# Kernel optimization log

Measured on AMD Instinct MI355X. Metric: run time of the kernel, lower is better.

## Reference

```python
import jax, jax.numpy as jnp
import numpy as np

B, T, F, H, L = 512, 512, 64, 128, 3


def setup_inputs() -> dict:
    key = jax.random.key(0)
    ks = jax.random.split(key, 6)
    s_in = 1.0 / np.sqrt(F)
    s_h = 1.0 / np.sqrt(H)
    return {
        "x": jax.random.normal(ks[0], (B, T, F), dtype=jnp.float32),
        "Wx0": jax.random.normal(ks[1], (F, 3 * H), dtype=jnp.float32) * s_in,
        "Wx_rest": jax.random.normal(ks[2], (L - 1, H, 3 * H), dtype=jnp.float32) * s_h,
        "Wh": jax.random.normal(ks[3], (L, H, 3 * H), dtype=jnp.float32) * s_h,
        "b": jnp.zeros((L, 3 * H), dtype=jnp.float32),
        "Wd": jax.random.normal(ks[4], (H, H), dtype=jnp.float32) * s_h,
        "bd": jnp.zeros((H,), dtype=jnp.float32),
    }


def _gru_layer(x_seq, Wx, Wh_l, b_l):
    """x_seq: [T, B, Din] -> [T, B, H]. Classic GRU (reset_after=False)."""
    # Precompute input projections for all timesteps in one GEMM: [T, B, 3H]
    gx = jnp.einsum("tbd,dg->tbg", x_seq, Wx) + b_l

    def step(h, gx_t):
        gh = h @ Wh_l                      # [B, 3H]
        xz, xr, xn = jnp.split(gx_t, 3, axis=-1)
        hz, hr, hn = jnp.split(gh, 3, axis=-1)
        z = jax.nn.sigmoid(xz + hz)
        r = jax.nn.sigmoid(xr + hr)
        n = jnp.tanh(xn + r * hn)
        h_new = z * h + (1.0 - z) * n
        return h_new, h_new

    h0 = jnp.zeros((x_seq.shape[1], Wh_l.shape[0]), dtype=x_seq.dtype)
    _, hs = jax.lax.scan(step, h0, gx)
    return hs                              # [T, B, H]


def reference(x, Wx0, Wx_rest, Wh, b, Wd, bd):
    h = jnp.swapaxes(x, 0, 1)              # [T, B, F] time-major for scan
    h = _gru_layer(h, Wx0, Wh[0], b[0])
    for l in range(1, L):                  # small fixed layer loop
        h = _gru_layer(h, Wx_rest[l - 1], Wh[l], b[l])
    h = jnp.swapaxes(h, 0, 1)              # [B, T, H]
    return jax.nn.sigmoid(jnp.einsum("bth,hk->btk", h, Wd) + bd)
```

## Files before the change

### kernel.cpp

```cpp
#include <hip/hip_runtime.h>

namespace {

constexpr int Bb = 512, Tt = 512, Ff = 64, Hh = 128, Gg = 384;
constexpr int CH = 64;
constexpr int NCH = Tt / CH;

using short8  = __attribute__((ext_vector_type(8))) short;
using short4v = __attribute__((ext_vector_type(4))) short;
using f32x4   = __attribute__((ext_vector_type(4))) float;

__device__ __forceinline__ short f2bf(float f) {
  unsigned u = __float_as_uint(f);
  u += 0x7FFFu + ((u >> 16) & 1u);
  return (short)(u >> 16);
}
__device__ __forceinline__ float bf2f(short s) {
  return __uint_as_float(((unsigned)(unsigned short)s) << 16);
}
__device__ __forceinline__ float sigm(float x) { return 1.0f / (1.0f + __expf(-x)); }
__device__ __forceinline__ float tanh_fast(float x) { return 1.0f - 2.0f / (1.0f + __expf(2.0f * x)); }

__device__ __forceinline__ void gl_lds16(const char* g, char* l) {
  __builtin_amdgcn_global_load_lds((const __attribute__((address_space(1))) void*)g,
                                   (__attribute__((address_space(3))) void*)l, 16, 0, 0);
}

__global__ __launch_bounds__(512, 4) void prep(const float* __restrict__ Wx0,
                                               const float* __restrict__ Wxr,
                                               const float* __restrict__ Wh,
                                               const float* __restrict__ Wd,
                                               char* __restrict__ WhF,
                                               char* __restrict__ WxF,
                                               char* __restrict__ WdF) {
  const int id = blockIdx.x * 512 + threadIdx.x;
  const int lane = id & 63, lr = lane & 15, lk = lane >> 4;
  const int q = id >> 6;
  const float* src; int col, ldn, row0; char* dst;
  if (q < 288) {
    const int l = q / 96, rem = q % 96, w = rem / 12, f = rem % 12;
    const int g = f >> 2, ks = f & 3;
    src = Wh + (size_t)l * Hh * Gg; ldn = Gg;
    col = g * 128 + w * 16 + lr; row0 = ks * 32 + lk * 8;
    dst = WhF + (size_t)(q * 64 + lane) * 16;
  } else if (q < 528) {
    int p = q - 288; int base;
    if (p < 48)       { src = Wx0; base = 0; }
    else if (p < 144) { src = Wxr; base = 48; p -= 48; }
    else              { src = Wxr + (size_t)Hh * Gg; base = 144; p -= 144; }
    int ct, ks;
    if (base == 0) { ct = p >> 1; ks = p & 1; } else { ct = p >> 2; ks = p & 3; }
    ldn = Gg; col = ct * 16 + lr; row0 = ks * 32 + lk * 8;
    dst = WxF + (size_t)((base + p) * 64 + lane) * 16;
  } else {
    const int p = q - 528;
    const int ct = p >> 2, ks = p & 3;
    src = Wd; ldn = Hh; col = ct * 16 + lr; row0 = ks * 32 + lk * 8;
    dst = WdF + (size_t)(p * 64 + lane) * 16;
  }
  short8 v;
#pragma unroll
  for (int j = 0; j < 8; ++j) v[j] = f2bf(src[(size_t)(row0 + j) * ldn + col]);
  *(short8*)dst = v;
}

template <int KS>
__device__ void gemm_chunk(const void* __restrict__ src, int t0,
                           const char* __restrict__ wxf,
                           const float* __restrict__ bias,
                           char* __restrict__ gx, int wg, char* at) {
  constexpr int ROWB = KS * 64;
  const int tid = threadIdx.x;
  const int w = tid >> 6, lane = tid & 63, lr = lane & 15, lk = lane >> 4;
  const int trel = wg >> 3, b0 = (wg & 7) * 64;

  if constexpr (KS == 2) {
    const float* x = (const float*)src;
    const int row = tid >> 3, seg = tid & 7;
    const float* pr = x + ((size_t)(b0 + row) * Tt + t0 + trel) * Ff + seg * 8;
    f32x4 a = *(const f32x4*)pr, c = *(const f32x4*)(pr + 4);
    short8 o;
#pragma unroll
    for (int j = 0; j < 4; ++j) { o[j] = f2bf(a[j]); o[4 + j] = f2bf(c[j]); }
    *(short8*)(at + row * ROWB + ((seg * 16) ^ ((row & 7) << 4))) = o;
  } else {
    const char* h = (const char*)src + ((size_t)trel * 512 + b0) * ROWB;
    gl_lds16(h + tid * 16, at + tid * 16);
    gl_lds16(h + 8192 + tid * 16, at + 8192 + tid * 16);
    asm volatile("s_waitcnt vmcnt(0)");
  }
  __syncthreads();

  short8 bw[3][KS];
  f32x4 bs4[3];
#pragma unroll
  for (int c = 0; c < 3; ++c) {
    const int ct = w * 3 + c;
    bs4[c] = *(const f32x4*)(bias + ct * 16 + lk * 4);
#pragma unroll
    for (int ks = 0; ks < KS; ++ks)
      bw[c][ks] = *(const short8*)(wxf + (size_t)((ct * KS + ks) * 64 + lane) * 16);
  }

#pragma unroll
  for (int rt = 0; rt < 4; ++rt) {
    const int row = rt * 16 + lr;
    short8 aa[KS];
#pragma unroll
    for (int ks = 0; ks < KS; ++ks)
      aa[ks] = *(const short8*)(at + row * ROWB + ((ks * 64 + lk * 16) ^ ((row & 7) << 4)));
#pragma unroll
    for (int c = 0; c < 3; ++c) {
      f32x4 acc = {0.f, 0.f, 0.f, 0.f};
#pragma unroll
      for (int ks = 0; ks < KS; ++ks)
        acc = __builtin_amdgcn_mfma_f32_16x16x32_bf16(bw[c][ks], aa[ks], acc, 0, 0, 0);
      const int ct = w * 3 + c;
      short4v o;
#pragma unroll
      for (int i = 0; i < 4; ++i) o[i] = f2bf(acc[i] + bs4[c][i]);
      const int rb = (b0 >> 4) + rt;
      *(short4v*)(gx + (size_t)((trel * 32 + rb) * 8 + (ct & 7)) * 1536 + lane * 24 + (ct >> 3) * 8) = o;
    }
  }
}

template <bool DENSE>
__device__ void scan_chunk(const char* __restrict__ gx,
                           const char* __restrict__ whf,
                           short* __restrict__ hstream,
                           float* __restrict__ state, int t0,
                           const char* __restrict__ wdf,
                           const float* __restrict__ bdp,
                           float* __restrict__ out, int rb,
                           char* h_buf, float* ob) {
  const int tid = threadIdx.x;
  const int w = tid >> 6, lane = tid & 63, lr = lane & 15, lk = lane >> 4;

  short8 bwh[3][4];
#pragma unroll
  for (int g = 0; g < 3; ++g)
#pragma unroll
    for (int ks = 0; ks < 4; ++ks)
      bwh[g][ks] = *(const short8*)(whf + (size_t)((w * 12 + g * 4 + ks) * 64 + lane) * 16);

  short8 bwd[4];
  f32x4 bd4 = {0.f, 0.f, 0.f, 0.f};
  if constexpr (DENSE) {
#pragma unroll
    for (int ks = 0; ks < 4; ++ks)
      bwd[ks] = *(const short8*)(wdf + (size_t)((w * 4 + ks) * 64 + lane) * 16);
    bd4 = *(const f32x4*)(bdp + w * 16 + lk * 4);
  }

  const int hoff = lr * 256 + (((w * 16 + lk * 4) * 2) ^ ((lr & 7) << 4));

  float hreg[4];
  if (t0 == 0) {
#pragma unroll
    for (int i = 0; i < 4; ++i) hreg[i] = 0.f;
    short* hz = (short*)h_buf;
    for (int i = tid; i < 2048; i += 512) hz[i] = 0;
  } else {
    f32x4 s = *(const f32x4*)(state + (size_t)(rb * 512 + tid) * 4);
    short4v sv;
#pragma unroll
    for (int i = 0; i < 4; ++i) { hreg[i] = s[i]; sv[i] = f2bf(s[i]); }
    *(short4v*)(h_buf + hoff) = sv;
  }

  auto issue = [&](int trel, short4v* d) {
    const char* p = gx + (size_t)((trel * 32 + rb) * 8 + w) * 1536 + lane * 24;
    d[0] = *(const short4v*)p;
    d[1] = *(const short4v*)(p + 8);
    d[2] = *(const short4v*)(p + 16);
  };
  short4v pfA[3], pfB[3];
  issue(0, pfA);
  issue(1, pfB);
  __syncthreads();

  auto step = [&](int t, short4v* cur) {
    const int pp = t & 1;
    char* const hsrc = h_buf + pp * 4096;
    char* const hdst = h_buf + (1 - pp) * 4096;

    const short4v g0 = cur[0], g1 = cur[1], g2 = cur[2];

    short8 ah[4];
#pragma unroll
    for (int ks = 0; ks < 4; ++ks)
      ah[ks] = *(const short8*)(hsrc + lr * 256 + ((ks * 64 + lk * 16) ^ ((lr & 7) << 4)));

    f32x4 aZ = {0.f, 0.f, 0.f, 0.f}, aR = aZ, aHn = aZ;
#pragma unroll
    for (int ks = 0; ks < 4; ++ks) {
      aZ  = __builtin_amdgcn_mfma_f32_16x16x32_bf16(bwh[0][ks], ah[ks], aZ, 0, 0, 0);
      aR  = __builtin_amdgcn_mfma_f32_16x16x32_bf16(bwh[1][ks], ah[ks], aR, 0, 0, 0);
      aHn = __builtin_amdgcn_mfma_f32_16x16x32_bf16(bwh[2][ks], ah[ks], aHn, 0, 0, 0);
    }
    if (t + 2 < t0 + CH) issue(t + 2 - t0, cur);

    if constexpr (DENSE) {
      if (t > 0) {
        f32x4 aD = {0.f, 0.f, 0.f, 0.f};
#pragma unroll
        for (int ks = 0; ks < 4; ++ks)
          aD = __builtin_amdgcn_mfma_f32_16x16x32_bf16(bwd[ks], ah[ks], aD, 0, 0, 0);
        f32x4 ov;
#pragma unroll
        for (int i = 0; i < 4; ++i) ov[i] = sigm(aD[i] + bd4[i]);
        *(f32x4*)(ob + pp * 2048 + lr * 128 + w * 16 + lk * 4) = ov;
      }
    }

    float hn4[4];
#pragma unroll
    for (int i = 0; i < 4; ++i) {
      const float z = sigm(aZ[i] + bf2f(g0[i]));
      const float r = sigm(aR[i] + bf2f(g1[i]));
      const float n = tanh_fast(bf2f(g2[i]) + r * aHn[i]);
      const float h = z * hreg[i] + (1.f - z) * n;
      hreg[i] = h;
      hn4[i] = h;
    }
    unsigned p01, p23;
    asm("v_cvt_pk_bf16_f32 %0, %1, %2" : "=v"(p01) : "v"(hn4[0]), "v"(hn4[1]));
    asm("v_cvt_pk_bf16_f32 %0, %1, %2" : "=v"(p23) : "v"(hn4[2]), "v"(hn4[3]));
    const unsigned long long hv64 = ((unsigned long long)p23 << 32) | p01;
    *(unsigned long long*)(hdst + hoff) = hv64;

    __builtin_amdgcn_sched_barrier(0);
    asm volatile("s_waitcnt lgkmcnt(0)");
    __builtin_amdgcn_s_barrier();
    __builtin_amdgcn_sched_barrier(0);

    if constexpr (DENSE) {
      if (t > 0) {
        f32x4 v = *(const f32x4*)(ob + pp * 2048 + tid * 4);
        *(f32x4*)(out + ((size_t)(rb * 16 + (tid >> 5)) * Tt + (t - 1)) * Hh + (tid & 31) * 4) = v;
      }
    } else {
      short4v hv = *(const short4v*)(hdst + tid * 8);
      *(short4v*)(hstream + (size_t)((t - t0) * 512 + rb * 16 + (tid >> 5)) * 128 + (tid & 31) * 4) = hv;
    }
  };

  for (int tb = t0; tb < t0 + CH; tb += 2) {
    step(tb, pfA);
    step(tb + 1, pfB);
  }

  {
    f32x4 sv;
#pragma unroll
    for (int i = 0; i < 4; ++i) sv[i] = hreg[i];
    *(f32x4*)(state + (size_t)(rb * 512 + tid) * 4) = sv;
  }

  if constexpr (DENSE) {
    if (t0 + CH == Tt) {
      short8 ah[4];
#pragma unroll
      for (int ks = 0; ks < 4; ++ks)
        ah[ks] = *(const short8*)(h_buf + lr * 256 + ((ks * 64 + lk * 16) ^ ((lr & 7) << 4)));
      f32x4 aD = {0.f, 0.f, 0.f, 0.f};
#pragma unroll
      for (int ks = 0; ks < 4; ++ks)
        aD = __builtin_amdgcn_mfma_f32_16x16x32_bf16(bwd[ks], ah[ks], aD, 0, 0, 0);
      f32x4 ov;
#pragma unroll
      for (int i = 0; i < 4; ++i) ov[i] = sigm(aD[i] + bd4[i]);
      *(f32x4*)(out + ((size_t)(rb * 16 + lr) * Tt + (Tt - 1)) * Hh + w * 16 + lk * 4) = ov;
    }
  }
}

struct GArgs { const void* src; char* gx; const char* wxf; const float* bias; int t0; int isx; };
struct SArgs { const char* gx; short* hstream; float* state; const char* whf; int t0; int dense; };

__global__ __launch_bounds__(512, 1) void gemm_multi(GArgs a0, GArgs a1, GArgs a2) {
  __shared__ char at[16384];
  const int g = blockIdx.x >> 9;
  const int wg = blockIdx.x & 511;
  GArgs a = (g == 0) ? a0 : (g == 1 ? a1 : a2);
  if (a.isx) gemm_chunk<2>(a.src, a.t0, a.wxf, a.bias, a.gx, wg, at);
  else       gemm_chunk<4>(a.src, a.t0, a.wxf, a.bias, a.gx, wg, at);
}

__global__ __launch_bounds__(512, 1) void scan_multi(SArgs a0, SArgs a1, SArgs a2,
                                                     const char* __restrict__ wdf,
                                                     const float* __restrict__ bd,
                                                     float* __restrict__ out) {
  __shared__ char hb[8192];
  __shared__ float ob[4096];
  const int g = blockIdx.x >> 5;
  const int rb = blockIdx.x & 31;
  SArgs a = (g == 0) ? a0 : (g == 1 ? a1 : a2);
  if (a.dense) scan_chunk<true >(a.gx, a.whf, a.hstream, a.state, a.t0, wdf, bd, out, rb, hb, ob);
  else         scan_chunk<false>(a.gx, a.whf, a.hstream, a.state, a.t0, wdf, bd, out, rb, hb, ob);
}

}

extern "C" void kernel_launch(void* const* d_in, const int* in_sizes, int n_in,
                              void* d_out, int out_size, void* d_ws, size_t ws_size,
                              hipStream_t stream) {
  const float* x   = (const float*)d_in[0];
  const float* Wx0 = (const float*)d_in[1];
  const float* Wxr = (const float*)d_in[2];
  const float* Wh  = (const float*)d_in[3];
  const float* b   = (const float*)d_in[4];
  const float* Wd  = (const float*)d_in[5];
  const float* bd  = (const float*)d_in[6];
  float* out = (float*)d_out;

  char* ws = (char*)d_ws;
  char*  WhF   = ws;
  char*  WxF   = ws + 294912;
  char*  WdF   = ws + 540672;
  float* state0 = (float*)(ws + 573440);
  float* state1 = state0 + 65536;
  float* state2 = state1 + 65536;
  char*  gx0 = ws + 2097152;
  char*  gx1 = gx0 + 25165824;
  char*  gx2 = gx1 + 25165824;
  char*  hc  = ws + 2097152 + 3 * 25165824;

  prep<<<70, 512, 0, stream>>>(Wx0, Wxr, Wh, Wd, WhF, WxF, WdF);

  const size_t WXOFF[3] = {0, 49152, 147456};
  for (int r = 0; r < NCH + 2; ++r) {
    GArgs ga[3]; SArgs sa[3]; int n = 0;
    for (int l = 0; l < 3; ++l) {
      const int k = r - l;
      if (k < 0 || k >= NCH) continue;
      const void* src = (l == 0) ? (const void*)x
                                 : (const void*)(hc + ((size_t)((l - 1) * 2 + (k & 1))) * 8388608);
      char*  gxl = (l == 0) ? gx0 : (l == 1 ? gx1 : gx2);
      float* st  = (l == 0) ? state0 : (l == 1 ? state1 : state2);
      ga[n] = { src, gxl, WxF + WXOFF[l], b + l * Gg, k * CH, l == 0 };
      sa[n] = { gxl, (l < 2) ? (short*)(hc + (size_t)(l * 2 + (k & 1)) * 8388608) : (short*)nullptr,
                st, WhF + (size_t)l * 98304, k * CH, l == 2 };
      ++n;
    }
    for (int i = n; i < 3; ++i) { ga[i] = ga[0]; sa[i] = sa[0]; }
    gemm_multi<<<n * 512, 512, 0, stream>>>(ga[0], ga[1], ga[2]);
    scan_multi<<<n * 32, 512, 0, stream>>>(sa[0], sa[1], sa[2], WdF, bd, out);
  }
}
```

Measured before the change: 1.151 ms.

## Process two row-blocks per scan workgroup with LDS counter sync instead of barrier

Each scan workgroup now advances two independent 16-row batches in lockstep, interleaving their MFMA chains to hide latency, and launches half as many blocks. The per-step s_barrier is replaced by LDS atomic counters that each wave increments and spin-waits on. The hidden-state stream store moves to the following step, and dense outputs go straight from registers to global memory without LDS staging. The aim is more instruction-level parallelism and cheaper synchronisation on the latency-bound recurrence. The cost is less block-level parallelism, more register pressure, and a bounded spin-wait that could quietly go wrong if it times out.

```diff
diff --git a/kernel.cpp b/kernel.cpp
--- a/kernel.cpp
+++ b/kernel.cpp
@@ -126,16 +126,17 @@
 }
 
 template <bool DENSE>
-__device__ void scan_chunk(const char* __restrict__ gx,
-                           const char* __restrict__ whf,
-                           short* __restrict__ hstream,
-                           float* __restrict__ state, int t0,
-                           const char* __restrict__ wdf,
-                           const float* __restrict__ bdp,
-                           float* __restrict__ out, int rb,
-                           char* h_buf, float* ob) {
+__device__ void scan_dual(const char* __restrict__ gx,
+                          const char* __restrict__ whf,
+                          short* __restrict__ hstream,
+                          float* __restrict__ state, int t0,
+                          const char* __restrict__ wdf,
+                          const float* __restrict__ bdp,
+                          float* __restrict__ out, int pb,
+                          char* hbA, char* hbB, int* cntA, int* cntB) {
   const int tid = threadIdx.x;
   const int w = tid >> 6, lane = tid & 63, lr = lane & 15, lk = lane >> 4;
+  const int rb0 = pb * 2, rb1 = pb * 2 + 1;
 
   short8 bwh[3][4];
 #pragma unroll
@@ -155,124 +156,175 @@
 
   const int hoff = lr * 256 + (((w * 16 + lk * 4) * 2) ^ ((lr & 7) << 4));
 
-  float hreg[4];
+  if (tid == 0) { *cntA = 0; *cntB = 0; }
+
+  float hrA[4], hrB[4];
   if (t0 == 0) {
 #pragma unroll
-    for (int i = 0; i < 4; ++i) hreg[i] = 0.f;
-    short* hz = (short*)h_buf;
-    for (int i = tid; i < 2048; i += 512) hz[i] = 0;
+    for (int i = 0; i < 4; ++i) { hrA[i] = 0.f; hrB[i] = 0.f; }
+    short* za = (short*)hbA;
+    short* zb = (short*)hbB;
+    for (int i = tid; i < 2048; i += 512) { za[i] = 0; zb[i] = 0; }
   } else {
-    f32x4 s = *(const f32x4*)(state + (size_t)(rb * 512 + tid) * 4);
-    short4v sv;
-#pragma unroll
-    for (int i = 0; i < 4; ++i) { hreg[i] = s[i]; sv[i] = f2bf(s[i]); }
-    *(short4v*)(h_buf + hoff) = sv;
-  }
-
-  auto issue = [&](int trel, short4v* d) {
+    f32x4 sA = *(const f32x4*)(state + (size_t)(rb0 * 512 + tid) * 4);
+    f32x4 sB = *(const f32x4*)(state + (size_t)(rb1 * 512 + tid) * 4);
+    short4v va, vb;
+#pragma unroll
+    for (int i = 0; i < 4; ++i) { hrA[i] = sA[i]; va[i] = f2bf(sA[i]);
+                                  hrB[i] = sB[i]; vb[i] = f2bf(sB[i]); }
+    *(short4v*)(hbA + hoff) = va;
+    *(short4v*)(hbB + hoff) = vb;
+  }
+
+  auto issue = [&](int rb, int trel, short4v* d) {
     const char* p = gx + (size_t)((trel * 32 + rb) * 8 + w) * 1536 + lane * 24;
     d[0] = *(const short4v*)p;
     d[1] = *(const short4v*)(p + 8);
     d[2] = *(const short4v*)(p + 16);
   };
-  short4v pfA[3], pfB[3];
-  issue(0, pfA);
-  issue(1, pfB);
+  short4v qA0[3], qA1[3], qB0[3], qB1[3];
+  issue(rb0, 0, qA0); issue(rb0, 1, qA1);
+  issue(rb1, 0, qB0); issue(rb1, 1, qB1);
   __syncthreads();
 
-  auto step = [&](int t, short4v* cur) {
-    const int pp = t & 1;
-    char* const hsrc = h_buf + pp * 4096;
-    char* const hdst = h_buf + (1 - pp) * 4096;
-
-    const short4v g0 = cur[0], g1 = cur[1], g2 = cur[2];
-
-    short8 ah[4];
-#pragma unroll
-    for (int ks = 0; ks < 4; ++ks)
-      ah[ks] = *(const short8*)(hsrc + lr * 256 + ((ks * 64 + lk * 16) ^ ((lr & 7) << 4)));
-
-    f32x4 aZ = {0.f, 0.f, 0.f, 0.f}, aR = aZ, aHn = aZ;
+  auto WAITP = [&](int* c, int target) {
+    int budget = 1 << 22;
+    while (__hip_atomic_load(c, __ATOMIC_RELAXED, __HIP_MEMORY_SCOPE_WORKGROUP) < target &&
+           --budget) {}
+  };
+
+  auto DUAL = [&](int t, short4v (&qA)[3], short4v (&qB)[3]) {
+    const int pin = t & 1;
+    const char* hsA = hbA + pin * 4096;
+    char* const hdA = hbA + (1 - pin) * 4096;
+    const char* hsB = hbB + pin * 4096;
+    char* const hdB = hbB + (1 - pin) * 4096;
+    const int tg = t0 + t;
+
+    if (t > 0) { WAITP(cntA, 8 * t); WAITP(cntB, 8 * t); }
+    __builtin_amdgcn_sched_barrier(0);
+
+    if (!DENSE && t > 0) {
+      short4v ha = *(const short4v*)(hsA + tid * 8);
+      short4v hb = *(const short4v*)(hsB + tid * 8);
+      *(short4v*)(hstream + ((size_t)(t - 1) * 512 + rb0 * 16 + (tid >> 5)) * 128 + (tid & 31) * 4) = ha;
+      *(short4v*)(hstream + ((size_t)(t - 1) * 512 + rb1 * 16 + (tid >> 5)) * 128 + (tid & 31) * 4) = hb;
+    }
+
+    const short4v a0 = qA[0], a1 = qA[1], a2 = qA[2];
+    const short4v b0 = qB[0], b1 = qB[1], b2 = qB[2];
+
+    short8 ahA[4], ahB[4];
 #pragma unroll
     for (int ks = 0; ks < 4; ++ks) {
-      aZ  = __builtin_amdgcn_mfma_f32_16x16x32_bf16(bwh[0][ks], ah[ks], aZ, 0, 0, 0);
-      aR  = __builtin_amdgcn_mfma_f32_16x16x32_bf16(bwh[1][ks], ah[ks], aR, 0, 0, 0);
-      aHn = __builtin_amdgcn_mfma_f32_16x16x32_bf16(bwh[2][ks], ah[ks], aHn, 0, 0, 0);
-    }
-    if (t + 2 < t0 + CH) issue(t + 2 - t0, cur);
+      const int off = lr * 256 + ((ks * 64 + lk * 16) ^ ((lr & 7) << 4));
+      ahA[ks] = *(const short8*)(hsA + off);
+      ahB[ks] = *(const short8*)(hsB + off);
+    }
+    if (t + 2 < CH) { issue(rb0, t + 2, qA); issue(rb1, t + 2, qB); }
+
+    f32x4 zA = {0.f, 0.f, 0.f, 0.f}, rA = zA, nA = zA;
+    f32x4 zB = zA, rB = zA, nB = zA;
+#pragma unroll
+    for (int ks = 0; ks < 4; ++ks) {
+      zA = __builtin_amdgcn_mfma_f32_16x16x32_bf16(bwh[0][ks], ahA[ks], zA, 0, 0, 0);
+      zB = __builtin_amdgcn_mfma_f32_16x16x32_bf16(bwh[0][ks], ahB[ks], zB, 0, 0, 0);
+      rA = __builtin_amdgcn_mfma_f32_16x16x32_bf16(bwh[1][ks], ahA[ks], rA, 0, 0, 0);
+      rB = __builtin_amdgcn_mfma_f32_16x16x32_bf16(bwh[1][ks], ahB[ks], rB, 0, 0, 0);
+      nA = __builtin_amdgcn_mfma_f32_16x16x32_bf16(bwh[2][ks], ahA[ks], nA, 0, 0, 0);
+      nB = __builtin_amdgcn_mfma_f32_16x16x32_bf16(bwh[2][ks], ahB[ks], nB, 0, 0, 0);
+    }
 
     if constexpr (DENSE) {
-      if (t > 0) {
-        f32x4 aD = {0.f, 0.f, 0.f, 0.f};
-#pragma unroll
-        for (int ks = 0; ks < 4; ++ks)
-          aD = __builtin_amdgcn_mfma_f32_16x16x32_bf16(bwd[ks], ah[ks], aD, 0, 0, 0);
-        f32x4 ov;
-#pragma unroll
-        for (int i = 0; i < 4; ++i) ov[i] = sigm(aD[i] + bd4[i]);
-        *(f32x4*)(ob + pp * 2048 + lr * 128 + w * 16 + lk * 4) = ov;
+      if (tg > 0) {
+        f32x4 dA = {0.f, 0.f, 0.f, 0.f}, dB = dA;
+#pragma unroll
+        for (int ks = 0; ks < 4; ++ks) {
+          dA = __builtin_amdgcn_mfma_f32_16x16x32_bf16(bwd[ks], ahA[ks], dA, 0, 0, 0);
+          dB = __builtin_amdgcn_mfma_f32_16x16x32_bf16(bwd[ks], ahB[ks], dB, 0, 0, 0);
+        }
+        f32x4 oA, oB;
+#pragma unroll
+        for (int i = 0; i < 4; ++i) { oA[i] = sigm(dA[i] + bd4[i]); oB[i] = sigm(dB[i] + bd4[i]); }
+        *(f32x4*)(out + ((size_t)(rb0 * 16 + lr) * Tt + (tg - 1)) * Hh + w * 16 + lk * 4) = oA;
+        *(f32x4*)(out + ((size_t)(rb1 * 16 + lr) * Tt + (tg - 1)) * Hh + w * 16 + lk * 4) = oB;
       }
     }
 
-    float hn4[4];
+    float hnA[4], hnB[4];
 #pragma unroll
     for (int i = 0; i < 4; ++i) {
-      const float z = sigm(aZ[i] + bf2f(g0[i]));
-      const float r = sigm(aR[i] + bf2f(g1[i]));
-      const float n = tanh_fast(bf2f(g2[i]) + r * aHn[i]);
-      const float h = z * hreg[i] + (1.f - z) * n;
-      hreg[i] = h;
-      hn4[i] = h;
-    }
-    unsigned p01, p23;
-    asm("v_cvt_pk_bf16_f32 %0, %1, %2" : "=v"(p01) : "v"(hn4[0]), "v"(hn4[1]));
-    asm("v_cvt_pk_bf16_f32 %0, %1, %2" : "=v"(p23) : "v"(hn4[2]), "v"(hn4[3]));
-    const unsigned long long hv64 = ((unsigned long long)p23 << 32) | p01;
-    *(unsigned long long*)(hdst + hoff) = hv64;
+      {
+        const float z = sigm(zA[i] + bf2f(a0[i]));
+        const float r = sigm(rA[i] + bf2f(a1[i]));
+        const float n = tanh_fast(bf2f(a2[i]) + r * nA[i]);
+        const float h = z * hrA[i] + (1.f - z) * n;
+        hrA[i] = h; hnA[i] = h;
+      }
+      {
+        const float z = sigm(zB[i] + bf2f(b0[i]));
+        const float r = sigm(rB[i] + bf2f(b1[i]));
+        const float n = tanh_fast(bf2f(b2[i]) + r * nB[i]);
+        const float h = z * hrB[i] + (1.f - z) * n;
+        hrB[i] = h; hnB[i] = h;
+      }
+    }
+    unsigned pa01, pa23, pb01, pb23;
+    asm("v_cvt_pk_bf16_f32 %0, %1, %2" : "=v"(pa01) : "v"(hnA[0]), "v"(hnA[1]));
+    asm("v_cvt_pk_bf16_f32 %0, %1, %2" : "=v"(pa23) : "v"(hnA[2]), "v"(hnA[3]));
+    asm("v_cvt_pk_bf16_f32 %0, %1, %2" : "=v"(pb01) : "v"(hnB[0]), "v"(hnB[1]));
+    asm("v_cvt_pk_bf16_f32 %0, %1, %2" : "=v"(pb23) : "v"(hnB[2]), "v"(hnB[3]));
+    *(unsigned long long*)(hdA + hoff) = ((unsigned long long)pa23 << 32) | pa01;
+    *(unsigned long long*)(hdB + hoff) = ((unsigned long long)pb23 << 32) | pb01;
 
     __builtin_amdgcn_sched_barrier(0);
     asm volatile("s_waitcnt lgkmcnt(0)");
-    __builtin_amdgcn_s_barrier();
     __builtin_amdgcn_sched_barrier(0);
-
-    if constexpr (DENSE) {
-      if (t > 0) {
-        f32x4 v = *(const f32x4*)(ob + pp * 2048 + tid * 4);
-        *(f32x4*)(out + ((size_t)(rb * 16 + (tid >> 5)) * Tt + (t - 1)) * Hh + (tid & 31) * 4) = v;
-      }
-    } else {
-      short4v hv = *(const short4v*)(hdst + tid * 8);
-      *(short4v*)(hstream + (size_t)((t - t0) * 512 + rb * 16 + (tid >> 5)) * 128 + (tid & 31) * 4) = hv;
-    }
+    if (lane == 0) { atomicAdd(cntA, 1); atomicAdd(cntB, 1); }
+    __builtin_amdgcn_sched_barrier(0);
   };
 
-  for (int tb = t0; tb < t0 + CH; tb += 2) {
-    step(tb, pfA);
-    step(tb + 1, pfB);
-  }
+  for (int tb = 0; tb < CH; tb += 2) {
+    DUAL(tb, qA0, qB0);
+    DUAL(tb + 1, qA1, qB1);
+  }
+
+  WAITP(cntA, 8 * CH);
+  WAITP(cntB, 8 * CH);
+  __builtin_amdgcn_sched_barrier(0);
 
   {
-    f32x4 sv;
-#pragma unroll
-    for (int i = 0; i < 4; ++i) sv[i] = hreg[i];
-    *(f32x4*)(state + (size_t)(rb * 512 + tid) * 4) = sv;
-  }
-
-  if constexpr (DENSE) {
-    if (t0 + CH == Tt) {
-      short8 ah[4];
-#pragma unroll
-      for (int ks = 0; ks < 4; ++ks)
-        ah[ks] = *(const short8*)(h_buf + lr * 256 + ((ks * 64 + lk * 16) ^ ((lr & 7) << 4)));
-      f32x4 aD = {0.f, 0.f, 0.f, 0.f};
-#pragma unroll
-      for (int ks = 0; ks < 4; ++ks)
-        aD = __builtin_amdgcn_mfma_f32_16x16x32_bf16(bwd[ks], ah[ks], aD, 0, 0, 0);
-      f32x4 ov;
-#pragma unroll
-      for (int i = 0; i < 4; ++i) ov[i] = sigm(aD[i] + bd4[i]);
-      *(f32x4*)(out + ((size_t)(rb * 16 + lr) * Tt + (Tt - 1)) * Hh + w * 16 + lk * 4) = ov;
-    }
+    f32x4 sA, sB;
+#pragma unroll
+    for (int i = 0; i < 4; ++i) { sA[i] = hrA[i]; sB[i] = hrB[i]; }
+    *(f32x4*)(state + (size_t)(rb0 * 512 + tid) * 4) = sA;
+    *(f32x4*)(state + (size_t)(rb1 * 512 + tid) * 4) = sB;
+  }
+
+  if constexpr (!DENSE) {
+    short4v ha = *(const short4v*)(hbA + tid * 8);
+    short4v hb = *(const short4v*)(hbB + tid * 8);
+    *(short4v*)(hstream + ((size_t)(CH - 1) * 512 + rb0 * 16 + (tid >> 5)) * 128 + (tid & 31) * 4) = ha;
+    *(short4v*)(hstream + ((size_t)(CH - 1) * 512 + rb1 * 16 + (tid >> 5)) * 128 + (tid & 31) * 4) = hb;
+  } else if (t0 + CH == Tt) {
+    short8 ahA[4], ahB[4];
+#pragma unroll
+    for (int ks = 0; ks < 4; ++ks) {
+      const int off = lr * 256 + ((ks * 64 + lk * 16) ^ ((lr & 7) << 4));
+      ahA[ks] = *(const short8*)(hbA + off);
+      ahB[ks] = *(const short8*)(hbB + off);
+    }
+    f32x4 dA = {0.f, 0.f, 0.f, 0.f}, dB = dA;
+#pragma unroll
+    for (int ks = 0; ks < 4; ++ks) {
+      dA = __builtin_amdgcn_mfma_f32_16x16x32_bf16(bwd[ks], ahA[ks], dA, 0, 0, 0);
+      dB = __builtin_amdgcn_mfma_f32_16x16x32_bf16(bwd[ks], ahB[ks], dB, 0, 0, 0);
+    }
+    f32x4 oA, oB;
+#pragma unroll
+    for (int i = 0; i < 4; ++i) { oA[i] = sigm(dA[i] + bd4[i]); oB[i] = sigm(dB[i] + bd4[i]); }
+    *(f32x4*)(out + ((size_t)(rb0 * 16 + lr) * Tt + (Tt - 1)) * Hh + w * 16 + lk * 4) = oA;
+    *(f32x4*)(out + ((size_t)(rb1 * 16 + lr) * Tt + (Tt - 1)) * Hh + w * 16 + lk * 4) = oB;
   }
 }
 
@@ -292,13 +344,15 @@
                                                      const char* __restrict__ wdf,
                                                      const float* __restrict__ bd,
                                                      float* __restrict__ out) {
-  __shared__ char hb[8192];
-  __shared__ float ob[4096];
-  const int g = blockIdx.x >> 5;
-  const int rb = blockIdx.x & 31;
+  __shared__ char hbA[8192], hbB[8192];
+  __shared__ int  cnt[2][16];
+  const int g = blockIdx.x >> 4;
+  const int pb = blockIdx.x & 15;
   SArgs a = (g == 0) ? a0 : (g == 1 ? a1 : a2);
-  if (a.dense) scan_chunk<true >(a.gx, a.whf, a.hstream, a.state, a.t0, wdf, bd, out, rb, hb, ob);
-  else         scan_chunk<false>(a.gx, a.whf, a.hstream, a.state, a.t0, wdf, bd, out, rb, hb, ob);
+  if (a.dense) scan_dual<true >(a.gx, a.whf, a.hstream, a.state, a.t0, wdf, bd, out,
+                                pb, hbA, hbB, &cnt[0][0], &cnt[1][0]);
+  else         scan_dual<false>(a.gx, a.whf, a.hstream, a.state, a.t0, wdf, bd, out,
+                                pb, hbA, hbB, &cnt[0][0], &cnt[1][0]);
 }
 
 }
@@ -346,6 +400,6 @@
     }
     for (int i = n; i < 3; ++i) { ga[i] = ga[0]; sa[i] = sa[0]; }
     gemm_multi<<<n * 512, 512, 0, stream>>>(ga[0], ga[1], ga[2]);
-    scan_multi<<<n * 32, 512, 0, stream>>>(sa[0], sa[1], sa[2], WdF, bd, out);
-  }
-}
+    scan_multi<<<n * 16, 512, 0, stream>>>(sa[0], sa[1], sa[2], WdF, bd, out);
+  }
+}
```

Measured after the change: 1.979 ms. +72.0%, slower.
